# Kernel optimization log

Measured on AMD Instinct MI355X. Metric: run time of the kernel, lower is better.

## Reference

```python
import jax, jax.numpy as jnp
import numpy as np

B, T, S = 64, 128, 128
E, H, D, K = 512, 1024, 1024, 1024  # embed, hidden, decoder_size, encoder.output_size
IN2 = 2 * D + 2 * H  # output_rnn input size


def gru_cell(x, h, Wih, Whh, bih, bhh):
    # PyTorch GRUCell math; gate order (r, z, n)
    gi = x @ Wih.T + bih
    gh = h @ Whh.T + bhh
    i_r, i_z, i_n = jnp.split(gi, 3, axis=-1)
    h_r, h_z, h_n = jnp.split(gh, 3, axis=-1)
    r = jax.nn.sigmoid(i_r + h_r)
    z = jax.nn.sigmoid(i_z + h_z)
    n = jnp.tanh(i_n + r * h_n)
    return (1.0 - z) * n + z * h


def setup_inputs() -> dict:
    key = jax.random.key(0)
    ks = jax.random.split(key, 24)
    p = 0.05
    rn = lambda k, s, sc=1.0: jax.random.normal(k, s, jnp.float32) * sc
    return {
        'reversed_input': rn(ks[0], (B, T, E)),
        'y_length': jnp.full((B,), T, jnp.int32),
        'mask': jnp.ones((B, T), bool),
        'y_states': rn(ks[1], (B, T, D)),
        'encoder_output': rn(ks[2], (B, S, K)),
        'src_mask': jnp.ones((B, 1, S), bool),
        # backward-reading GRU (self.rnn)
        'rnn_Wih': rn(ks[3], (3 * H, E), p), 'rnn_Whh': rn(ks[4], (3 * H, H), p),
        'rnn_bih': rn(ks[5], (3 * H,), p), 'rnn_bhh': rn(ks[6], (3 * H,), p),
        # output_rnn GRU
        'out_Wih': rn(ks[7], (3 * H, IN2), p), 'out_Whh': rn(ks[8], (3 * H, H), p),
        'out_bih': rn(ks[9], (3 * H,), p), 'out_bhh': rn(ks[10], (3 * H,), p),
        'corr_W': rn(ks[11], (D, H), p), 'corr_b': rn(ks[12], (D,), p),
        'reward_W': rn(ks[13], (2, H), p), 'reward_b': rn(ks[14], (2,), p),
        'attv_W': rn(ks[15], (H, H + K), p), 'attv_b': rn(ks[16], (H,), p),
        # Bahdanau attention (bias-free linears)
        'key_W': rn(ks[17], (H, K), p), 'query_W': rn(ks[18], (H, H), p),
        'energy_W': rn(ks[19], (1, H), p),
    }


def reference(reversed_input, y_length, mask, y_states, encoder_output, src_mask,
              rnn_Wih, rnn_Whh, rnn_bih, rnn_bhh,
              out_Wih, out_Whh, out_bih, out_bhh,
              corr_W, corr_b, reward_W, reward_b,
              attv_W, attv_b, key_W, query_W, energy_W):
    b, t, _ = reversed_input.shape
    h_dim = rnn_Whh.shape[1]
    d_dim = corr_W.shape[0]
    dt = reversed_input.dtype

    # _apply_rnn: step-by-step GRU over reversed input == full GRU scan
    def rnn_step(h, x):
        h = gru_cell(x, h, rnn_Wih, rnn_Whh, rnn_bih, rnn_bhh)
        return h, h
    h0 = jnp.zeros((b, h_dim), dt)
    _, rnn_outs = jax.lax.scan(rnn_step, h0, reversed_input.transpose(1, 0, 2))
    rnn_outputs = jnp.flip(rnn_outs.transpose(1, 0, 2), axis=1)  # [B,T,H]

    proj_keys = encoder_output @ key_W.T  # [B,S,H] precomputed attention keys
    comb_states = jnp.concatenate([y_states, rnn_outputs], axis=-1)  # [B,T,D+H]
    sm = src_mask[:, 0, :]  # [B,S]

    def step(carry, comb_t):
        h, corr_prev, att_prev = carry
        inp = jnp.concatenate([comb_t, corr_prev, att_prev], axis=-1)  # [B,2D+2H]
        h = gru_cell(inp, h, out_Wih, out_Whh, out_bih, out_bhh)  # rnn_output == hidden[-1]
        corr = jnp.tanh(h @ corr_W.T + corr_b)  # corr_activation=tanh
        reward = h @ reward_W.T + reward_b  # [B,2]
        reward_pred = jax.lax.stop_gradient(jnp.argmax(reward, axis=-1)).astype(dt)[:, None]
        # Bahdanau attention: v^T tanh(Wq q + Wk k)
        pq = h @ query_W.T  # [B,H]
        energies = jnp.tanh(pq[:, None, :] + proj_keys) @ energy_W[0]  # [B,S]
        scores = jnp.where(sm, energies, -jnp.inf)
        alphas = jax.nn.softmax(scores, axis=-1)
        context = jnp.einsum('bs,bsk->bk', alphas, encoder_output)
        att_vec = jnp.tanh(jnp.concatenate([h, context], axis=-1) @ attv_W.T + attv_b)
        corr = corr * (1.0 - reward_pred)
        return (h, corr, att_vec), (corr, reward, alphas)

    init = (jnp.zeros((b, h_dim), dt), jnp.zeros((b, d_dim), dt), jnp.zeros((b, h_dim), dt))
    _, (corrs, rewards, attns) = jax.lax.scan(step, init, comb_states.transpose(1, 0, 2))
    return (corrs.transpose(1, 0, 2), rewards.transpose(1, 0, 2), attns.transpose(1, 0, 2))
```

## Files before the change

### kernel.cpp

```cpp
#include <hip/hip_runtime.h>
#include <hip/hip_bf16.h>
#include <math.h>

#define B 64
#define T 128
#define S 128
#define E 512
#define H 1024
#define D 1024
#define KDIM 1024
#define G3 3072
#define JT 16

__device__ __forceinline__ float sigmoidf_(float x) { return 1.f / (1.f + expf(-x)); }

template<int SRC>
__global__ __launch_bounds__(256) void gemm128(
    const float* __restrict__ A1, const float* __restrict__ A2, int lda,
    const float* __restrict__ W, int ldw, const float* __restrict__ bias,
    float* __restrict__ C, int ldc, int Kd, int c0, int chLog) {
  __shared__ __align__(16) float As[16][132];
  __shared__ __align__(16) float Ws[16][132];
  const int bm = blockIdx.y * 128;
  const int bn = blockIdx.x * 128;
  const int tid = threadIdx.x;
  const int tr = tid >> 4, tc = tid & 15;
  float acc[8][8];
#pragma unroll
  for (int i = 0; i < 8; ++i)
#pragma unroll
    for (int j = 0; j < 8; ++j) acc[i][j] = 0.f;

  for (int k0 = 0; k0 < Kd; k0 += 16) {
#pragma unroll
    for (int l = 0; l < 8; ++l) {
      int i = tid + l * 256;
      int r = i >> 4, kk = i & 15;
      int rg = bm + r;
      int k = k0 + kk;
      float v;
      if (SRC == 0) {
        v = A1[(size_t)rg * lda + k];
      } else {
        int b = rg >> chLog, tl = rg & ((1 << chLog) - 1);
        int trow = b * T + c0 + tl;
        if (SRC == 1) v = A1[(size_t)trow * E + k];
        else v = (k < 1024) ? A1[(size_t)trow * 1024 + k]
                            : A2[(size_t)trow * 1024 + (k - 1024)];
      }
      As[kk][r] = v;
    }
#pragma unroll
    for (int l = 0; l < 8; ++l) {
      int i = tid + l * 256;
      int c = i >> 4, kk = i & 15;
      Ws[kk][c] = W[(size_t)(bn + c) * ldw + k0 + kk];
    }
    __syncthreads();
#pragma unroll
    for (int kk = 0; kk < 16; ++kk) {
      float a[8], w[8];
      *(float4*)&a[0] = *(const float4*)&As[kk][tr * 8];
      *(float4*)&a[4] = *(const float4*)&As[kk][tr * 8 + 4];
      *(float4*)&w[0] = *(const float4*)&Ws[kk][tc * 8];
      *(float4*)&w[4] = *(const float4*)&Ws[kk][tc * 8 + 4];
#pragma unroll
      for (int i = 0; i < 8; ++i)
#pragma unroll
        for (int j = 0; j < 8; ++j)
          acc[i][j] = fmaf(a[i], w[j], acc[i][j]);
    }
    __syncthreads();
  }
#pragma unroll
  for (int i = 0; i < 8; ++i) {
    int rg = bm + tr * 8 + i;
#pragma unroll
    for (int j = 0; j < 8; ++j) {
      int cc = bn + tc * 8 + j;
      float bv = bias ? bias[cc] : 0.f;
      C[(size_t)rg * ldc + cc] = acc[i][j] + bv;
    }
  }
}

struct SBSeg { const float* A; const float* W; int lda; int ldw; int N; };
struct SBArgs { SBSeg s[6]; };

__global__ __launch_bounds__(256) void sb_gemm(SBArgs args, int jtPerSeg, int Nstr,
                                               float* __restrict__ part) {
  const int seg = blockIdx.x / jtPerSeg;
  const int jt = blockIdx.x % jtPerSeg;
  const SBSeg sg = args.s[seg];
  const int j0 = jt * JT;
  if (j0 >= sg.N) return;
  const int wv = __builtin_amdgcn_readfirstlane(threadIdx.x >> 6);
  const int lane = threadIdx.x & 63;
  float a[128];
  const float4* ap = (const float4*)(sg.A + (size_t)lane * sg.lda + wv * 128);
#pragma unroll
  for (int q = 0; q < 32; ++q) {
    float4 v = ap[q];
    a[q * 4 + 0] = v.x; a[q * 4 + 1] = v.y; a[q * 4 + 2] = v.z; a[q * 4 + 3] = v.w;
  }
  float acc[JT];
#pragma unroll
  for (int jj = 0; jj < JT; ++jj) acc[jj] = 0.f;
#pragma unroll
  for (int jj = 0; jj < JT; ++jj) {
    int j = j0 + jj;
    if (j < sg.N) {
      const float4* wp = (const float4*)(sg.W + (size_t)j * sg.ldw + wv * 128);
      float s0 = 0.f, s1 = 0.f, s2 = 0.f, s3 = 0.f;
#pragma unroll
      for (int q = 0; q < 32; ++q) {
        float4 w4 = wp[q];
        s0 = fmaf(a[q * 4 + 0], w4.x, s0);
        s1 = fmaf(a[q * 4 + 1], w4.y, s1);
        s2 = fmaf(a[q * 4 + 2], w4.z, s2);
        s3 = fmaf(a[q * 4 + 3], w4.w, s3);
      }
      acc[jj] = (s0 + s1) + (s2 + s3);
    }
  }
  __shared__ float red[4][JT][64];
#pragma unroll
  for (int jj = 0; jj < JT; ++jj) red[wv][jj][lane] = acc[jj];
  __syncthreads();
  for (int idx = threadIdx.x; idx < JT * 64; idx += 256) {
    int b = idx >> 4, jj = idx & 15;
    int j = j0 + jj;
    if (j < sg.N) {
      float v = red[0][jj][b] + red[1][jj][b] + red[2][jj][b] + red[3][jj][b];
      part[((size_t)seg * 64 + b) * Nstr + j] = v;
    }
  }
}

__global__ __launch_bounds__(256) void gru_reduce(
    const float* __restrict__ part, const float* __restrict__ gi,
    int CH, int tl, int nsGi, int ghStart, int nsGh,
    const float* __restrict__ bhh, float* __restrict__ hrow,
    float* __restrict__ flip_out, int t) {
  const int b = blockIdx.x >> 2;
  const int j = (blockIdx.x & 3) * 256 + threadIdx.x;
  const float* gb = gi + (size_t)(b * CH + tl) * G3;
  float gir = gb[j];
  float giz = gb[H + j];
  float gin = gb[2 * H + j];
  for (int p2 = 0; p2 < nsGi; ++p2) {
    const float* pp = part + ((size_t)p2 * 64 + b) * G3;
    gir += pp[j]; giz += pp[H + j]; gin += pp[2 * H + j];
  }
  float ghr = bhh[j], ghz = bhh[H + j], ghn = bhh[2 * H + j];
  for (int p2 = ghStart; p2 < ghStart + nsGh; ++p2) {
    const float* pp = part + ((size_t)p2 * 64 + b) * G3;
    ghr += pp[j]; ghz += pp[H + j]; ghn += pp[2 * H + j];
  }
  float r = sigmoidf_(gir + ghr);
  float z = sigmoidf_(giz + ghz);
  float n = tanhf(gin + r * ghn);
  float hold = hrow[(size_t)b * H + j];
  float hnew = (1.f - z) * n + z * hold;
  hrow[(size_t)b * H + j] = hnew;
  if (flip_out)
    flip_out[(size_t)b * T * H + (size_t)(T - 1 - t) * H + j] = hnew;
}

__global__ __launch_bounds__(256) void hproj_gemm(
    const float* __restrict__ h,
    const float* __restrict__ corrW, const float* __restrict__ corrB,
    const float* __restrict__ qW, const float* __restrict__ avW,
    const float* __restrict__ rewW, const float* __restrict__ rewB,
    float* __restrict__ corrR, float* __restrict__ pq,
    float* __restrict__ attH, float* __restrict__ rew,
    float* __restrict__ out_rewards, int t) {
  const int task = blockIdx.x;
  const int tid = threadIdx.x;
  const int wv = __builtin_amdgcn_readfirstlane(tid >> 6);
  const int lane = tid & 63;
  const float* Wb; int ldw = 1024, n0, nrows, typ;
  if (task < 128)      { Wb = corrW; n0 = task * 8;         nrows = 8; typ = 0; }
  else if (task < 256) { Wb = qW;    n0 = (task - 128) * 8; nrows = 8; typ = 1; }
  else if (task < 384) { Wb = avW;   n0 = (task - 256) * 8; nrows = 8; typ = 2; ldw = 2048; }
  else                 { Wb = rewW;  n0 = 0;                nrows = 2; typ = 3; }
  const int k0 = wv * 256;
  const float* arow = h + (size_t)lane * H + k0;
  float acc[8] = {0.f, 0.f, 0.f, 0.f, 0.f, 0.f, 0.f, 0.f};
  for (int sc = 0; sc < 8; ++sc) {
    float av[32];
    const float4* ap = (const float4*)(arow + sc * 32);
#pragma unroll
    for (int q = 0; q < 8; ++q) {
      float4 v = ap[q];
      av[4*q] = v.x; av[4*q+1] = v.y; av[4*q+2] = v.z; av[4*q+3] = v.w;
    }
#pragma unroll
    for (int rr = 0; rr < 8; ++rr) {
      if (rr < nrows) {
        const float4* wp = (const float4*)(Wb + (size_t)(n0 + rr) * ldw + k0 + sc * 32);
        float s = acc[rr];
#pragma unroll
        for (int q = 0; q < 8; ++q) {
          float4 w = wp[q];
          s = fmaf(av[4*q],   w.x, s);
          s = fmaf(av[4*q+1], w.y, s);
          s = fmaf(av[4*q+2], w.z, s);
          s = fmaf(av[4*q+3], w.w, s);
        }
        acc[rr] = s;
      }
    }
  }
  __shared__ float red[4][8][64];
#pragma unroll
  for (int rr = 0; rr < 8; ++rr) red[wv][rr][lane] = acc[rr];
  __syncthreads();
  for (int idx = tid; idx < 512; idx += 256) {
    int b = idx >> 3, jj = idx & 7;
    if (jj < nrows) {
      int n = n0 + jj;
      float v = red[0][jj][b] + red[1][jj][b] + red[2][jj][b] + red[3][jj][b];
      if (typ == 0) corrR[(size_t)b * 1024 + n] = v + corrB[n];
      else if (typ == 1) pq[(size_t)b * 1024 + n] = v;
      else if (typ == 2) attH[(size_t)n * 64 + b] = v;
      else {
        float rv = v + rewB[n];
        rew[n * 64 + b] = rv;
        out_rewards[((size_t)b * T + t) * 2 + n] = rv;
      }
    }
  }
}

__global__ __launch_bounds__(256) void energy_kernel(
    const float* __restrict__ pq, const float* __restrict__ pk,
    const float* __restrict__ eW, float* __restrict__ energies) {
  int wid = blockIdx.x * 4 + (threadIdx.x >> 6);
  int lane = threadIdx.x & 63;
  int b = wid >> 7, s = wid & 127;
  const float* pkp = pk + ((size_t)b * S + s) * H;
  const float* qp = pq + (size_t)b * H;
  float acc = 0.f;
#pragma unroll
  for (int i = 0; i < 16; ++i) {
    int j = lane + i * 64;
    acc += tanhf(qp[j] + pkp[j]) * eW[j];
  }
#pragma unroll
  for (int off = 32; off > 0; off >>= 1) acc += __shfl_down(acc, off);
  if (lane == 0) energies[b * S + s] = acc;
}

__global__ __launch_bounds__(256) void smct_plus(
    const float* __restrict__ energies, const float* __restrict__ enc,
    const float* __restrict__ corrR, const float* __restrict__ rew,
    float* __restrict__ ctx, float* __restrict__ uv,
    float* __restrict__ out_attns, float* __restrict__ out_corrs, int t) {
  int b = blockIdx.x, kt = blockIdx.y;
  int tid = threadIdx.x;
  __shared__ float se[128], sa[128], ss[128];
  if (tid < 128) { se[tid] = energies[b * S + tid]; sa[tid] = se[tid]; }
  __syncthreads();
  for (int st2 = 64; st2 > 0; st2 >>= 1) {
    if (tid < st2) sa[tid] = fmaxf(sa[tid], sa[tid + st2]);
    __syncthreads();
  }
  float mx = sa[0];
  __syncthreads();
  if (tid < 128) { sa[tid] = expf(se[tid] - mx); ss[tid] = sa[tid]; }
  __syncthreads();
  for (int st2 = 64; st2 > 0; st2 >>= 1) {
    if (tid < st2) ss[tid] += ss[tid + st2];
    __syncthreads();
  }
  float inv = 1.f / ss[0];
  __syncthreads();
  if (tid < 128) sa[tid] *= inv;
  __syncthreads();
  int k = kt * 256 + tid;
  const float* eb = enc + (size_t)b * S * KDIM + k;
  float acc = 0.f;
#pragma unroll 4
  for (int s2 = 0; s2 < S; ++s2) acc = fmaf(sa[s2], eb[(size_t)s2 * KDIM], acc);
  ctx[(size_t)b * KDIM + k] = acc;
  float r0 = rew[b], r1 = rew[64 + b];
  float g = (r1 > r0) ? 0.f : 1.f;
  float cv = g * tanhf(corrR[(size_t)b * 1024 + k]);
  uv[(size_t)b * 2048 + k] = cv;
  out_corrs[((size_t)b * T + t) * D + k] = cv;
  if (kt == 0 && tid < 128) out_attns[((size_t)b * T + t) * S + tid] = sa[tid];
}

__global__ __launch_bounds__(256) void final_attv(
    const float* __restrict__ attH, const float* __restrict__ avW,
    const float* __restrict__ avB, const float* __restrict__ ctx,
    float* __restrict__ uv) {
  const int n0 = blockIdx.x * 8;
  const int tid = threadIdx.x;
  const int wv = __builtin_amdgcn_readfirstlane(tid >> 6);
  const int lane = tid & 63;
  __shared__ float red[4][8][64];
  float acc[8];
#pragma unroll
  for (int jj = 0; jj < 8; ++jj) acc[jj] = 0.f;
  const int k0 = wv * 256;
  const float* arow = ctx + (size_t)lane * KDIM + k0;
  for (int sc = 0; sc < 8; ++sc) {
    float av[32];
    const float4* ap = (const float4*)(arow + sc * 32);
#pragma unroll
    for (int q = 0; q < 8; ++q) {
      float4 v = ap[q];
      av[4*q] = v.x; av[4*q+1] = v.y; av[4*q+2] = v.z; av[4*q+3] = v.w;
    }
#pragma unroll
    for (int jj = 0; jj < 8; ++jj) {
      const float4* wp = (const float4*)(avW + (size_t)(n0 + jj) * 2048 + 1024 + k0 + sc * 32);
      float s = acc[jj];
#pragma unroll
      for (int q = 0; q < 8; ++q) {
        float4 w = wp[q];
        s = fmaf(av[4*q],   w.x, s);
        s = fmaf(av[4*q+1], w.y, s);
        s = fmaf(av[4*q+2], w.z, s);
        s = fmaf(av[4*q+3], w.w, s);
      }
      acc[jj] = s;
    }
  }
#pragma unroll
  for (int jj = 0; jj < 8; ++jj) red[wv][jj][lane] = acc[jj];
  __syncthreads();
  for (int idx = tid; idx < 512; idx += 256) {
    int jj = idx >> 6, bb = idx & 63;
    int n = n0 + jj;
    float v = red[0][jj][bb] + red[1][jj][bb] + red[2][jj][bb] + red[3][jj][bb]
            + attH[(size_t)n * 64 + bb] + avB[n];
    uv[(size_t)bb * 2048 + 1024 + n] = tanhf(v);
  }
}

extern "C" void kernel_launch(void* const* d_in, const int* in_sizes, int n_in,
                              void* d_out, int out_size, void* d_ws, size_t ws_size,
                              hipStream_t stream) {
  const float* reversed_input = (const float*)d_in[0];
  const float* y_states = (const float*)d_in[3];
  const float* encoder = (const float*)d_in[4];
  const float* rnn_Wih = (const float*)d_in[6];
  const float* rnn_Whh = (const float*)d_in[7];
  const float* rnn_bih = (const float*)d_in[8];
  const float* rnn_bhh = (const float*)d_in[9];
  const float* out_Wih = (const float*)d_in[10];
  const float* out_Whh = (const float*)d_in[11];
  const float* out_bih = (const float*)d_in[12];
  const float* out_bhh = (const float*)d_in[13];
  const float* corr_W = (const float*)d_in[14];
  const float* corr_b = (const float*)d_in[15];
  const float* reward_W = (const float*)d_in[16];
  const float* reward_b = (const float*)d_in[17];
  const float* attv_W = (const float*)d_in[18];
  const float* attv_b = (const float*)d_in[19];
  const float* key_W = (const float*)d_in[20];
  const float* query_W = (const float*)d_in[21];
  const float* energy_W = (const float*)d_in[22];

  float* out_corrs = (float*)d_out;
  float* out_rewards = out_corrs + (size_t)B * T * D;
  float* out_attns = out_rewards + (size_t)B * T * 2;

  float* p = (float*)d_ws;
  float* rnn_flip = p;  p += (size_t)B * T * H;
  float* proj_keys = p; p += (size_t)B * S * H;
  float* part = p;      p += (size_t)6 * 64 * G3;
  float* h = p;         p += (size_t)B * H;
  float* uv = p;        p += (size_t)B * 2048;
  float* ctx = p;       p += (size_t)B * KDIM;
  float* corrR = p;     p += (size_t)B * 1024;
  float* pq = p;        p += (size_t)B * H;
  float* attH = p;      p += (size_t)H * 64;
  float* rew = p;       p += 128;
  float* energ = p;     p += (size_t)B * S;
  size_t fixedF = (size_t)(p - (float*)d_ws);
  int CH = 8, chLog = 3;
  {
    int c = 64, l = 6;
    for (; c >= 8; c >>= 1, --l)
      if (ws_size >= (fixedF + (size_t)c * 64 * G3) * 4) break;
    if (c < 8) { c = 8; l = 3; }
    CH = c; chLog = l;
  }
  float* gibuf = p;

  hipMemsetAsync(h, 0, (size_t)B * H * sizeof(float), stream);
  hipMemsetAsync(uv, 0, (size_t)B * 2048 * sizeof(float), stream);

  dim3 blk(256);

  gemm128<0><<<dim3(H / 128, (B * S) / 128), blk, 0, stream>>>(
      encoder, nullptr, KDIM, key_W, KDIM, nullptr, proj_keys, H, KDIM, 0, 0);

  for (int c0 = 0; c0 < T; c0 += CH) {
    gemm128<1><<<dim3(G3 / 128, (64 * CH) / 128), blk, 0, stream>>>(
        reversed_input, nullptr, 0, rnn_Wih, E, rnn_bih, gibuf, G3, E, c0, chLog);
    for (int tl = 0; tl < CH; ++tl) {
      int t = c0 + tl;
      SBArgs s1{};
      s1.s[0] = { h, rnn_Whh, H, H, G3 };
      s1.s[1] = { h + 512, rnn_Whh + 512, H, H, G3 };
      sb_gemm<<<2 * 192, blk, 0, stream>>>(s1, 192, G3, part);
      gru_reduce<<<256, blk, 0, stream>>>(part, gibuf, CH, tl, 0, 0, 2,
                                          rnn_bhh, h, rnn_flip, t);
    }
  }

  hipMemsetAsync(h, 0, (size_t)B * H * sizeof(float), stream);
  for (int c0 = 0; c0 < T; c0 += CH) {
    gemm128<2><<<dim3(G3 / 128, (64 * CH) / 128), blk, 0, stream>>>(
        y_states, rnn_flip, 0, out_Wih, 4096, out_bih, gibuf, G3, 2048, c0, chLog);
    for (int tl = 0; tl < CH; ++tl) {
      int t = c0 + tl;
      SBArgs k1{};
      for (int s2 = 0; s2 < 4; ++s2)
        k1.s[s2] = { uv + s2 * 512, out_Wih + 2048 + s2 * 512, 2048, 4096, G3 };
      for (int s2 = 0; s2 < 2; ++s2)
        k1.s[4 + s2] = { h + s2 * 512, out_Whh + s2 * 512, H, H, G3 };
      sb_gemm<<<6 * 192, blk, 0, stream>>>(k1, 192, G3, part);
      gru_reduce<<<256, blk, 0, stream>>>(part, gibuf, CH, tl, 4, 4, 2,
                                          out_bhh, h, nullptr, t);
      hproj_gemm<<<385, blk, 0, stream>>>(h, corr_W, corr_b, query_W, attv_W,
                                          reward_W, reward_b, corrR, pq, attH,
                                          rew, out_rewards, t);
      energy_kernel<<<2048, blk, 0, stream>>>(pq, proj_keys, energy_W, energ);
      smct_plus<<<dim3(B, 4), blk, 0, stream>>>(energ, encoder, corrR, rew,
                                                ctx, uv, out_attns, out_corrs, t);
      final_attv<<<128, blk, 0, stream>>>(attH, attv_W, attv_b, ctx, uv);
    }
  }
}
```

Baseline: 23.03 ms.

## Fuse GRU reduction and softmax-context into producer kernels via last-block atomics

Merges the split-K recurrent GEMM with the GRU gate reduction in one kernel. An atomic counter per column group lets the last finishing block compute the gates, and the hidden state is double-buffered to avoid read/write races. The energy kernel and the softmax/context kernel are fused the same way, with a per-batch counter. This removes two launches per timestep. In exchange, the final reduction and the context computation now run on only a few blocks (one per batch row for context), so that tail work is serialized.

```diff
diff --git a/kernel.cpp b/kernel.cpp
--- a/kernel.cpp
+++ b/kernel.cpp
@@ -84,87 +84,100 @@
   }
 }
 
-struct SBSeg { const float* A; const float* W; int lda; int ldw; int N; };
-struct SBArgs { SBSeg s[6]; };
-
-__global__ __launch_bounds__(256) void sb_gemm(SBArgs args, int jtPerSeg, int Nstr,
-                                               float* __restrict__ part) {
-  const int seg = blockIdx.x / jtPerSeg;
-  const int jt = blockIdx.x % jtPerSeg;
-  const SBSeg sg = args.s[seg];
+struct SBSeg { const float* A; const float* W; int lda; int ldw; };
+struct FGArgs {
+  SBSeg s[6];
+  int nseg;
+  int nsGi;
+  const float* gi;
+  int CH; int tl;
+  const float* bhh;
+  const float* hprev;
+  float* hcur;
+  float* flip;
+  int t;
+  float* part;
+  unsigned int* cnt;
+};
+
+__global__ __launch_bounds__(256) void sbg_gru(FGArgs a) {
+  const int seg = blockIdx.x / 192;
+  const int jt = blockIdx.x % 192;
+  const SBSeg sg = a.s[seg];
   const int j0 = jt * JT;
-  if (j0 >= sg.N) return;
-  const int wv = __builtin_amdgcn_readfirstlane(threadIdx.x >> 6);
-  const int lane = threadIdx.x & 63;
-  float a[128];
+  const int tid = threadIdx.x;
+  const int wv = __builtin_amdgcn_readfirstlane(tid >> 6);
+  const int lane = tid & 63;
+  float av[128];
   const float4* ap = (const float4*)(sg.A + (size_t)lane * sg.lda + wv * 128);
 #pragma unroll
   for (int q = 0; q < 32; ++q) {
     float4 v = ap[q];
-    a[q * 4 + 0] = v.x; a[q * 4 + 1] = v.y; a[q * 4 + 2] = v.z; a[q * 4 + 3] = v.w;
+    av[q * 4 + 0] = v.x; av[q * 4 + 1] = v.y; av[q * 4 + 2] = v.z; av[q * 4 + 3] = v.w;
   }
   float acc[JT];
 #pragma unroll
   for (int jj = 0; jj < JT; ++jj) acc[jj] = 0.f;
 #pragma unroll
   for (int jj = 0; jj < JT; ++jj) {
-    int j = j0 + jj;
-    if (j < sg.N) {
-      const float4* wp = (const float4*)(sg.W + (size_t)j * sg.ldw + wv * 128);
-      float s0 = 0.f, s1 = 0.f, s2 = 0.f, s3 = 0.f;
-#pragma unroll
-      for (int q = 0; q < 32; ++q) {
-        float4 w4 = wp[q];
-        s0 = fmaf(a[q * 4 + 0], w4.x, s0);
-        s1 = fmaf(a[q * 4 + 1], w4.y, s1);
-        s2 = fmaf(a[q * 4 + 2], w4.z, s2);
-        s3 = fmaf(a[q * 4 + 3], w4.w, s3);
-      }
-      acc[jj] = (s0 + s1) + (s2 + s3);
-    }
+    const float4* wp = (const float4*)(sg.W + (size_t)(j0 + jj) * sg.ldw + wv * 128);
+    float s0 = 0.f, s1 = 0.f, s2 = 0.f, s3 = 0.f;
+#pragma unroll
+    for (int q = 0; q < 32; ++q) {
+      float4 w4 = wp[q];
+      s0 = fmaf(av[q * 4 + 0], w4.x, s0);
+      s1 = fmaf(av[q * 4 + 1], w4.y, s1);
+      s2 = fmaf(av[q * 4 + 2], w4.z, s2);
+      s3 = fmaf(av[q * 4 + 3], w4.w, s3);
+    }
+    acc[jj] = (s0 + s1) + (s2 + s3);
   }
   __shared__ float red[4][JT][64];
 #pragma unroll
   for (int jj = 0; jj < JT; ++jj) red[wv][jj][lane] = acc[jj];
   __syncthreads();
-  for (int idx = threadIdx.x; idx < JT * 64; idx += 256) {
+  for (int idx = tid; idx < JT * 64; idx += 256) {
     int b = idx >> 4, jj = idx & 15;
-    int j = j0 + jj;
-    if (j < sg.N) {
-      float v = red[0][jj][b] + red[1][jj][b] + red[2][jj][b] + red[3][jj][b];
-      part[((size_t)seg * 64 + b) * Nstr + j] = v;
-    }
-  }
-}
-
-__global__ __launch_bounds__(256) void gru_reduce(
-    const float* __restrict__ part, const float* __restrict__ gi,
-    int CH, int tl, int nsGi, int ghStart, int nsGh,
-    const float* __restrict__ bhh, float* __restrict__ hrow,
-    float* __restrict__ flip_out, int t) {
-  const int b = blockIdx.x >> 2;
-  const int j = (blockIdx.x & 3) * 256 + threadIdx.x;
-  const float* gb = gi + (size_t)(b * CH + tl) * G3;
-  float gir = gb[j];
-  float giz = gb[H + j];
-  float gin = gb[2 * H + j];
-  for (int p2 = 0; p2 < nsGi; ++p2) {
-    const float* pp = part + ((size_t)p2 * 64 + b) * G3;
-    gir += pp[j]; giz += pp[H + j]; gin += pp[2 * H + j];
-  }
-  float ghr = bhh[j], ghz = bhh[H + j], ghn = bhh[2 * H + j];
-  for (int p2 = ghStart; p2 < ghStart + nsGh; ++p2) {
-    const float* pp = part + ((size_t)p2 * 64 + b) * G3;
-    ghr += pp[j]; ghz += pp[H + j]; ghn += pp[2 * H + j];
-  }
-  float r = sigmoidf_(gir + ghr);
-  float z = sigmoidf_(giz + ghz);
-  float n = tanhf(gin + r * ghn);
-  float hold = hrow[(size_t)b * H + j];
-  float hnew = (1.f - z) * n + z * hold;
-  hrow[(size_t)b * H + j] = hnew;
-  if (flip_out)
-    flip_out[(size_t)b * T * H + (size_t)(T - 1 - t) * H + j] = hnew;
+    float v = red[0][jj][b] + red[1][jj][b] + red[2][jj][b] + red[3][jj][b];
+    a.part[((size_t)seg * 64 + b) * G3 + j0 + jj] = v;
+  }
+  __threadfence();
+  __syncthreads();
+  __shared__ int isLast;
+  if (tid == 0) {
+    int grp = jt & 63;
+    unsigned int old = atomicAdd(&a.cnt[grp], 1u);
+    isLast = (old == (unsigned)(a.nseg * 3 - 1)) ? 1 : 0;
+    if (isLast) a.cnt[grp] = 0;
+  }
+  __syncthreads();
+  if (!isLast) return;
+  __threadfence();
+  const int grp = jt & 63;
+  const int jg0 = grp * 16;
+  for (int idx = tid; idx < 1024; idx += 256) {
+    int b = idx >> 4, jj = idx & 15;
+    int j = jg0 + jj;
+    const float* gb = a.gi + (size_t)(b * a.CH + a.tl) * G3;
+    float gir = gb[j], giz = gb[H + j], gin = gb[2 * H + j];
+    for (int p2 = 0; p2 < a.nsGi; ++p2) {
+      const float* pp = a.part + ((size_t)p2 * 64 + b) * G3;
+      gir += pp[j]; giz += pp[H + j]; gin += pp[2 * H + j];
+    }
+    float ghr = a.bhh[j], ghz = a.bhh[H + j], ghn = a.bhh[2 * H + j];
+    for (int p2 = a.nsGi; p2 < a.nseg; ++p2) {
+      const float* pp = a.part + ((size_t)p2 * 64 + b) * G3;
+      ghr += pp[j]; ghz += pp[H + j]; ghn += pp[2 * H + j];
+    }
+    float r = sigmoidf_(gir + ghr);
+    float z = sigmoidf_(giz + ghz);
+    float n = tanhf(gin + r * ghn);
+    float hold = a.hprev[(size_t)b * H + j];
+    float hnew = (1.f - z) * n + z * hold;
+    a.hcur[(size_t)b * H + j] = hnew;
+    if (a.flip)
+      a.flip[(size_t)b * T * H + (size_t)(T - 1 - a.t) * H + j] = hnew;
+  }
 }
 
 __global__ __launch_bounds__(256) void hproj_gemm(
@@ -233,34 +246,45 @@
   }
 }
 
-__global__ __launch_bounds__(256) void energy_kernel(
+__global__ __launch_bounds__(256) void energy_smct(
     const float* __restrict__ pq, const float* __restrict__ pk,
-    const float* __restrict__ eW, float* __restrict__ energies) {
-  int wid = blockIdx.x * 4 + (threadIdx.x >> 6);
-  int lane = threadIdx.x & 63;
-  int b = wid >> 7, s = wid & 127;
-  const float* pkp = pk + ((size_t)b * S + s) * H;
-  const float* qp = pq + (size_t)b * H;
-  float acc = 0.f;
-#pragma unroll
-  for (int i = 0; i < 16; ++i) {
-    int j = lane + i * 64;
-    acc += tanhf(qp[j] + pkp[j]) * eW[j];
-  }
-#pragma unroll
-  for (int off = 32; off > 0; off >>= 1) acc += __shfl_down(acc, off);
-  if (lane == 0) energies[b * S + s] = acc;
-}
-
-__global__ __launch_bounds__(256) void smct_plus(
-    const float* __restrict__ energies, const float* __restrict__ enc,
+    const float* __restrict__ eW, const float* __restrict__ enc,
     const float* __restrict__ corrR, const float* __restrict__ rew,
     float* __restrict__ ctx, float* __restrict__ uv,
+    float* __restrict__ energ, unsigned int* __restrict__ cnt,
     float* __restrict__ out_attns, float* __restrict__ out_corrs, int t) {
-  int b = blockIdx.x, kt = blockIdx.y;
-  int tid = threadIdx.x;
-  __shared__ float se[128], sa[128], ss[128];
-  if (tid < 128) { se[tid] = energies[b * S + tid]; sa[tid] = se[tid]; }
+  const int tid = threadIdx.x;
+  const int wv = tid >> 6, lane = tid & 63;
+  const int wid = blockIdx.x * 4 + wv;
+  const int b = blockIdx.x >> 5;
+  {
+    const int s = wid & 127;
+    const float* pkp = pk + ((size_t)b * S + s) * H;
+    const float* qp = pq + (size_t)b * H;
+    float acc = 0.f;
+#pragma unroll
+    for (int i = 0; i < 16; ++i) {
+      int j = lane + i * 64;
+      acc += tanhf(qp[j] + pkp[j]) * eW[j];
+    }
+#pragma unroll
+    for (int off = 32; off > 0; off >>= 1) acc += __shfl_down(acc, off);
+    if (lane == 0) energ[b * S + s] = acc;
+  }
+  __threadfence();
+  __syncthreads();
+  __shared__ int isLast;
+  if (tid == 0) {
+    unsigned int old = atomicAdd(&cnt[b], 1u);
+    isLast = (old == 31u) ? 1 : 0;
+    if (isLast) cnt[b] = 0;
+  }
+  __syncthreads();
+  if (!isLast) return;
+  __threadfence();
+  __shared__ float sa[128], ss[128];
+  float ev = 0.f;
+  if (tid < 128) { ev = energ[b * S + tid]; sa[tid] = ev; }
   __syncthreads();
   for (int st2 = 64; st2 > 0; st2 >>= 1) {
     if (tid < st2) sa[tid] = fmaxf(sa[tid], sa[tid + st2]);
@@ -268,7 +292,8 @@
   }
   float mx = sa[0];
   __syncthreads();
-  if (tid < 128) { sa[tid] = expf(se[tid] - mx); ss[tid] = sa[tid]; }
+  float e2 = 0.f;
+  if (tid < 128) { e2 = expf(ev - mx); sa[tid] = e2; ss[tid] = e2; }
   __syncthreads();
   for (int st2 = 64; st2 > 0; st2 >>= 1) {
     if (tid < st2) ss[tid] += ss[tid + st2];
@@ -276,20 +301,26 @@
   }
   float inv = 1.f / ss[0];
   __syncthreads();
-  if (tid < 128) sa[tid] *= inv;
-  __syncthreads();
-  int k = kt * 256 + tid;
-  const float* eb = enc + (size_t)b * S * KDIM + k;
-  float acc = 0.f;
-#pragma unroll 4
-  for (int s2 = 0; s2 < S; ++s2) acc = fmaf(sa[s2], eb[(size_t)s2 * KDIM], acc);
-  ctx[(size_t)b * KDIM + k] = acc;
+  if (tid < 128) {
+    float a2 = e2 * inv;
+    sa[tid] = a2;
+    out_attns[((size_t)b * T + t) * S + tid] = a2;
+  }
+  __syncthreads();
   float r0 = rew[b], r1 = rew[64 + b];
   float g = (r1 > r0) ? 0.f : 1.f;
-  float cv = g * tanhf(corrR[(size_t)b * 1024 + k]);
-  uv[(size_t)b * 2048 + k] = cv;
-  out_corrs[((size_t)b * T + t) * D + k] = cv;
-  if (kt == 0 && tid < 128) out_attns[((size_t)b * T + t) * S + tid] = sa[tid];
+#pragma unroll
+  for (int kq = 0; kq < 4; ++kq) {
+    int k = kq * 256 + tid;
+    const float* eb = enc + (size_t)b * S * KDIM + k;
+    float acc = 0.f;
+#pragma unroll 4
+    for (int s2 = 0; s2 < S; ++s2) acc = fmaf(sa[s2], eb[(size_t)s2 * KDIM], acc);
+    ctx[(size_t)b * KDIM + k] = acc;
+    float cv = g * tanhf(corrR[(size_t)b * 1024 + k]);
+    uv[(size_t)b * 2048 + k] = cv;
+    out_corrs[((size_t)b * T + t) * D + k] = cv;
+  }
 }
 
 __global__ __launch_bounds__(256) void final_attv(
@@ -373,7 +404,8 @@
   float* rnn_flip = p;  p += (size_t)B * T * H;
   float* proj_keys = p; p += (size_t)B * S * H;
   float* part = p;      p += (size_t)6 * 64 * G3;
-  float* h = p;         p += (size_t)B * H;
+  float* hA = p;        p += (size_t)B * H;
+  float* hB = p;        p += (size_t)B * H;
   float* uv = p;        p += (size_t)B * 2048;
   float* ctx = p;       p += (size_t)B * KDIM;
   float* corrR = p;     p += (size_t)B * 1024;
@@ -381,6 +413,8 @@
   float* attH = p;      p += (size_t)H * 64;
   float* rew = p;       p += 128;
   float* energ = p;     p += (size_t)B * S;
+  unsigned int* cntG = (unsigned int*)p; p += 64;
+  unsigned int* cntB = (unsigned int*)p; p += 64;
   size_t fixedF = (size_t)(p - (float*)d_ws);
   int CH = 8, chLog = 3;
   {
@@ -392,8 +426,9 @@
   }
   float* gibuf = p;
 
-  hipMemsetAsync(h, 0, (size_t)B * H * sizeof(float), stream);
+  hipMemsetAsync(hA, 0, (size_t)B * H * sizeof(float), stream);
   hipMemsetAsync(uv, 0, (size_t)B * 2048 * sizeof(float), stream);
+  hipMemsetAsync(cntG, 0, 128 * sizeof(unsigned int), stream);
 
   dim3 blk(256);
 
@@ -405,35 +440,45 @@
         reversed_input, nullptr, 0, rnn_Wih, E, rnn_bih, gibuf, G3, E, c0, chLog);
     for (int tl = 0; tl < CH; ++tl) {
       int t = c0 + tl;
-      SBArgs s1{};
-      s1.s[0] = { h, rnn_Whh, H, H, G3 };
-      s1.s[1] = { h + 512, rnn_Whh + 512, H, H, G3 };
-      sb_gemm<<<2 * 192, blk, 0, stream>>>(s1, 192, G3, part);
-      gru_reduce<<<256, blk, 0, stream>>>(part, gibuf, CH, tl, 0, 0, 2,
-                                          rnn_bhh, h, rnn_flip, t);
-    }
-  }
-
-  hipMemsetAsync(h, 0, (size_t)B * H * sizeof(float), stream);
+      const float* hp_ = (t & 1) ? hB : hA;
+      float* hc_ = (t & 1) ? hA : hB;
+      FGArgs fa{};
+      fa.s[0] = { hp_, rnn_Whh, H, H };
+      fa.s[1] = { hp_ + 512, rnn_Whh + 512, H, H };
+      fa.nseg = 2; fa.nsGi = 0;
+      fa.gi = gibuf; fa.CH = CH; fa.tl = tl;
+      fa.bhh = rnn_bhh; fa.hprev = hp_; fa.hcur = hc_;
+      fa.flip = rnn_flip; fa.t = t;
+      fa.part = part; fa.cnt = cntG;
+      sbg_gru<<<2 * 192, blk, 0, stream>>>(fa);
+    }
+  }
+
+  hipMemsetAsync(hA, 0, (size_t)B * H * sizeof(float), stream);
   for (int c0 = 0; c0 < T; c0 += CH) {
     gemm128<2><<<dim3(G3 / 128, (64 * CH) / 128), blk, 0, stream>>>(
         y_states, rnn_flip, 0, out_Wih, 4096, out_bih, gibuf, G3, 2048, c0, chLog);
     for (int tl = 0; tl < CH; ++tl) {
       int t = c0 + tl;
-      SBArgs k1{};
+      const float* hp_ = (t & 1) ? hB : hA;
+      float* hc_ = (t & 1) ? hA : hB;
+      FGArgs fa{};
       for (int s2 = 0; s2 < 4; ++s2)
-        k1.s[s2] = { uv + s2 * 512, out_Wih + 2048 + s2 * 512, 2048, 4096, G3 };
+        fa.s[s2] = { uv + s2 * 512, out_Wih + 2048 + s2 * 512, 2048, 4096 };
       for (int s2 = 0; s2 < 2; ++s2)
-        k1.s[4 + s2] = { h + s2 * 512, out_Whh + s2 * 512, H, H, G3 };
-      sb_gemm<<<6 * 192, blk, 0, stream>>>(k1, 192, G3, part);
-      gru_reduce<<<256, blk, 0, stream>>>(part, gibuf, CH, tl, 4, 4, 2,
-                                          out_bhh, h, nullptr, t);
-      hproj_gemm<<<385, blk, 0, stream>>>(h, corr_W, corr_b, query_W, attv_W,
+        fa.s[4 + s2] = { hp_ + s2 * 512, out_Whh + s2 * 512, H, H };
+      fa.nseg = 6; fa.nsGi = 4;
+      fa.gi = gibuf; fa.CH = CH; fa.tl = tl;
+      fa.bhh = out_bhh; fa.hprev = hp_; fa.hcur = hc_;
+      fa.flip = nullptr; fa.t = t;
+      fa.part = part; fa.cnt = cntG;
+      sbg_gru<<<6 * 192, blk, 0, stream>>>(fa);
+      hproj_gemm<<<385, blk, 0, stream>>>(hc_, corr_W, corr_b, query_W, attv_W,
                                           reward_W, reward_b, corrR, pq, attH,
                                           rew, out_rewards, t);
-      energy_kernel<<<2048, blk, 0, stream>>>(pq, proj_keys, energy_W, energ);
-      smct_plus<<<dim3(B, 4), blk, 0, stream>>>(energ, encoder, corrR, rew,
-                                                ctx, uv, out_attns, out_corrs, t);
+      energy_smct<<<2048, blk, 0, stream>>>(pq, proj_keys, energy_W, encoder,
+                                            corrR, rew, ctx, uv, energ, cntB,
+                                            out_attns, out_corrs, t);
       final_attv<<<128, blk, 0, stream>>>(attH, attv_W, attv_b, ctx, uv);
     }
   }
```

New measurement: 68.73 ms. +198.5%, slower.

## Fuse first GRU matvec with gate update; merge energy into attention kernel

Applied to the files above, without the earlier changes.

The backward-reading GRU step now runs as a single 512-thread kernel that computes h@Whh for four hidden units across all batches, reduces across waves in shared memory, and applies the gate math directly. It ping-pongs between two hidden-state buffers, which replaces the two launches and the partial-sum round trip through global memory. The energy computation is folded into the softmax/context kernel, dropping a launch and the energies buffer. The cost is that each of the 4 k-slice blocks per batch now recomputes all 128 energies redundantly, and the fused GRU kernel reads Whh with less parallelism per block.

```diff
diff --git a/kernel.cpp b/kernel.cpp
--- a/kernel.cpp
+++ b/kernel.cpp
@@ -81,6 +81,75 @@
       float bv = bias ? bias[cc] : 0.f;
       C[(size_t)rg * ldc + cc] = acc[i][j] + bv;
     }
+  }
+}
+
+struct G1Args {
+  const float* gi; const float* Whh; const float* bhh;
+  const float* hprev; float* hcur; float* flip;
+  int CH; int tl; int t;
+};
+
+__global__ __launch_bounds__(512) void fused_g1(G1Args a) {
+  const int j0 = blockIdx.x * 4;
+  const int tid = threadIdx.x;
+  const int wv = tid >> 6, lane = tid & 63;
+  __shared__ float red[8][12][64];
+  __shared__ float st[4][64];
+  float acc[12];
+#pragma unroll
+  for (int r = 0; r < 12; ++r) acc[r] = 0.f;
+  for (int p = 0; p < 2; ++p) {
+    const int k0 = (p * 8 + wv) * 64;
+    float av[64];
+    const float4* ap = (const float4*)(a.hprev + (size_t)lane * H + k0);
+#pragma unroll
+    for (int q = 0; q < 16; ++q) {
+      float4 v = ap[q];
+      av[4*q] = v.x; av[4*q+1] = v.y; av[4*q+2] = v.z; av[4*q+3] = v.w;
+    }
+#pragma unroll
+    for (int jj = 0; jj < 4; ++jj)
+#pragma unroll
+      for (int g = 0; g < 3; ++g) {
+        const float4* wp = (const float4*)(a.Whh + (size_t)(g * H + j0 + jj) * H + k0);
+        float s = acc[jj * 3 + g];
+#pragma unroll
+        for (int q = 0; q < 16; ++q) {
+          float4 w = wp[q];
+          s = fmaf(av[4*q],   w.x, s);
+          s = fmaf(av[4*q+1], w.y, s);
+          s = fmaf(av[4*q+2], w.z, s);
+          s = fmaf(av[4*q+3], w.w, s);
+        }
+        acc[jj * 3 + g] = s;
+      }
+  }
+#pragma unroll
+  for (int r = 0; r < 12; ++r) red[wv][r][lane] = acc[r];
+  __syncthreads();
+  if (tid < 256) {
+    const int jj = tid >> 6, b = tid & 63, j = j0 + jj;
+    float ghr = a.bhh[j], ghz = a.bhh[H + j], ghn = a.bhh[2 * H + j];
+#pragma unroll
+    for (int w = 0; w < 8; ++w) {
+      ghr += red[w][jj * 3 + 0][b];
+      ghz += red[w][jj * 3 + 1][b];
+      ghn += red[w][jj * 3 + 2][b];
+    }
+    const float* gb = a.gi + (size_t)(b * a.CH + a.tl) * G3;
+    float r = sigmoidf_(gb[j] + ghr);
+    float z = sigmoidf_(gb[H + j] + ghz);
+    float n = tanhf(gb[2 * H + j] + r * ghn);
+    float hnew = (1.f - z) * n + z * a.hprev[(size_t)b * H + j];
+    st[jj][b] = hnew;
+  }
+  __syncthreads();
+  if (tid < 256) {
+    const int jl = tid & 3, b2 = tid >> 2;
+    float v = st[jl][b2];
+    a.hcur[(size_t)b2 * H + j0 + jl] = v;
+    a.flip[(size_t)b2 * T * H + (size_t)(T - 1 - a.t) * H + j0 + jl] = v;
   }
 }
 
@@ -233,34 +302,37 @@
   }
 }
 
-__global__ __launch_bounds__(256) void energy_kernel(
+__global__ __launch_bounds__(256) void attn_slice(
     const float* __restrict__ pq, const float* __restrict__ pk,
-    const float* __restrict__ eW, float* __restrict__ energies) {
-  int wid = blockIdx.x * 4 + (threadIdx.x >> 6);
-  int lane = threadIdx.x & 63;
-  int b = wid >> 7, s = wid & 127;
-  const float* pkp = pk + ((size_t)b * S + s) * H;
-  const float* qp = pq + (size_t)b * H;
-  float acc = 0.f;
-#pragma unroll
-  for (int i = 0; i < 16; ++i) {
-    int j = lane + i * 64;
-    acc += tanhf(qp[j] + pkp[j]) * eW[j];
-  }
-#pragma unroll
-  for (int off = 32; off > 0; off >>= 1) acc += __shfl_down(acc, off);
-  if (lane == 0) energies[b * S + s] = acc;
-}
-
-__global__ __launch_bounds__(256) void smct_plus(
-    const float* __restrict__ energies, const float* __restrict__ enc,
+    const float* __restrict__ eW, const float* __restrict__ enc,
     const float* __restrict__ corrR, const float* __restrict__ rew,
     float* __restrict__ ctx, float* __restrict__ uv,
     float* __restrict__ out_attns, float* __restrict__ out_corrs, int t) {
-  int b = blockIdx.x, kt = blockIdx.y;
-  int tid = threadIdx.x;
+  const int b = blockIdx.x;
+  const int ks = blockIdx.y;
+  const int tid = threadIdx.x;
+  const int s = tid & 127, half = tid >> 7;
+  __shared__ float ep[2][128];
   __shared__ float se[128], sa[128], ss[128];
-  if (tid < 128) { se[tid] = energies[b * S + tid]; sa[tid] = se[tid]; }
+  {
+    const float4* qp = (const float4*)(pq + (size_t)b * H + half * 512);
+    const float4* pkp = (const float4*)(pk + ((size_t)b * S + s) * H + half * 512);
+    const float4* ewp = (const float4*)(eW + half * 512);
+    float acc = 0.f;
+#pragma unroll 4
+    for (int q = 0; q < 128; ++q) {
+      float4 qv = qp[q];
+      float4 kv = pkp[q];
+      float4 evv = ewp[q];
+      acc += tanhf(qv.x + kv.x) * evv.x;
+      acc += tanhf(qv.y + kv.y) * evv.y;
+      acc += tanhf(qv.z + kv.z) * evv.z;
+      acc += tanhf(qv.w + kv.w) * evv.w;
+    }
+    ep[half][s] = acc;
+  }
+  __syncthreads();
+  if (tid < 128) { float e = ep[0][tid] + ep[1][tid]; se[tid] = e; sa[tid] = e; }
   __syncthreads();
   for (int st2 = 64; st2 > 0; st2 >>= 1) {
     if (tid < st2) sa[tid] = fmaxf(sa[tid], sa[tid + st2]);
@@ -268,7 +340,7 @@
   }
   float mx = sa[0];
   __syncthreads();
-  if (tid < 128) { sa[tid] = expf(se[tid] - mx); ss[tid] = sa[tid]; }
+  if (tid < 128) { float e2 = expf(se[tid] - mx); sa[tid] = e2; ss[tid] = e2; }
   __syncthreads();
   for (int st2 = 64; st2 > 0; st2 >>= 1) {
     if (tid < st2) ss[tid] += ss[tid + st2];
@@ -278,7 +350,8 @@
   __syncthreads();
   if (tid < 128) sa[tid] *= inv;
   __syncthreads();
-  int k = kt * 256 + tid;
+  if (ks == 0 && tid < 128) out_attns[((size_t)b * T + t) * S + tid] = sa[tid];
+  const int k = ks * 256 + tid;
   const float* eb = enc + (size_t)b * S * KDIM + k;
   float acc = 0.f;
 #pragma unroll 4
@@ -289,7 +362,6 @@
   float cv = g * tanhf(corrR[(size_t)b * 1024 + k]);
   uv[(size_t)b * 2048 + k] = cv;
   out_corrs[((size_t)b * T + t) * D + k] = cv;
-  if (kt == 0 && tid < 128) out_attns[((size_t)b * T + t) * S + tid] = sa[tid];
 }
 
 __global__ __launch_bounds__(256) void final_attv(
@@ -373,14 +445,14 @@
   float* rnn_flip = p;  p += (size_t)B * T * H;
   float* proj_keys = p; p += (size_t)B * S * H;
   float* part = p;      p += (size_t)6 * 64 * G3;
-  float* h = p;         p += (size_t)B * H;
+  float* hA = p;        p += (size_t)B * H;
+  float* hB = p;        p += (size_t)B * H;
   float* uv = p;        p += (size_t)B * 2048;
   float* ctx = p;       p += (size_t)B * KDIM;
   float* corrR = p;     p += (size_t)B * 1024;
   float* pq = p;        p += (size_t)B * H;
   float* attH = p;      p += (size_t)H * 64;
   float* rew = p;       p += 128;
-  float* energ = p;     p += (size_t)B * S;
   size_t fixedF = (size_t)(p - (float*)d_ws);
   int CH = 8, chLog = 3;
   {
@@ -392,10 +464,10 @@
   }
   float* gibuf = p;
 
-  hipMemsetAsync(h, 0, (size_t)B * H * sizeof(float), stream);
+  hipMemsetAsync(hA, 0, (size_t)B * H * sizeof(float), stream);
   hipMemsetAsync(uv, 0, (size_t)B * 2048 * sizeof(float), stream);
 
-  dim3 blk(256);
+  dim3 blk(256), blk512(512);
 
   gemm128<0><<<dim3(H / 128, (B * S) / 128), blk, 0, stream>>>(
       encoder, nullptr, KDIM, key_W, KDIM, nullptr, proj_keys, H, KDIM, 0, 0);
@@ -405,16 +477,16 @@
         reversed_input, nullptr, 0, rnn_Wih, E, rnn_bih, gibuf, G3, E, c0, chLog);
     for (int tl = 0; tl < CH; ++tl) {
       int t = c0 + tl;
-      SBArgs s1{};
-      s1.s[0] = { h, rnn_Whh, H, H, G3 };
-      s1.s[1] = { h + 512, rnn_Whh + 512, H, H, G3 };
-      sb_gemm<<<2 * 192, blk, 0, stream>>>(s1, 192, G3, part);
-      gru_reduce<<<256, blk, 0, stream>>>(part, gibuf, CH, tl, 0, 0, 2,
-                                          rnn_bhh, h, rnn_flip, t);
-    }
-  }
-
-  hipMemsetAsync(h, 0, (size_t)B * H * sizeof(float), stream);
+      G1Args g1;
+      g1.gi = gibuf; g1.Whh = rnn_Whh; g1.bhh = rnn_bhh;
+      g1.hprev = (t & 1) ? hB : hA;
+      g1.hcur = (t & 1) ? hA : hB;
+      g1.flip = rnn_flip; g1.CH = CH; g1.tl = tl; g1.t = t;
+      fused_g1<<<256, blk512, 0, stream>>>(g1);
+    }
+  }
+
+  hipMemsetAsync(hA, 0, (size_t)B * H * sizeof(float), stream);
   for (int c0 = 0; c0 < T; c0 += CH) {
     gemm128<2><<<dim3(G3 / 128, (64 * CH) / 128), blk, 0, stream>>>(
         y_states, rnn_flip, 0, out_Wih, 4096, out_bih, gibuf, G3, 2048, c0, chLog);
@@ -424,16 +496,16 @@
       for (int s2 = 0; s2 < 4; ++s2)
         k1.s[s2] = { uv + s2 * 512, out_Wih + 2048 + s2 * 512, 2048, 4096, G3 };
       for (int s2 = 0; s2 < 2; ++s2)
-        k1.s[4 + s2] = { h + s2 * 512, out_Whh + s2 * 512, H, H, G3 };
+        k1.s[4 + s2] = { hA + s2 * 512, out_Whh + s2 * 512, H, H, G3 };
       sb_gemm<<<6 * 192, blk, 0, stream>>>(k1, 192, G3, part);
       gru_reduce<<<256, blk, 0, stream>>>(part, gibuf, CH, tl, 4, 4, 2,
-                                          out_bhh, h, nullptr, t);
-      hproj_gemm<<<385, blk, 0, stream>>>(h, corr_W, corr_b, query_W, attv_W,
+                                          out_bhh, hA, nullptr, t);
+      hproj_gemm<<<385, blk, 0, stream>>>(hA, corr_W, corr_b, query_W, attv_W,
                                           reward_W, reward_b, corrR, pq, attH,
                                           rew, out_rewards, t);
-      energy_kernel<<<2048, blk, 0, stream>>>(pq, proj_keys, energy_W, energ);
-      smct_plus<<<dim3(B, 4), blk, 0, stream>>>(energ, encoder, corrR, rew,
-                                                ctx, uv, out_attns, out_corrs, t);
+      attn_slice<<<dim3(B, 4), blk, 0, stream>>>(pq, proj_keys, energy_W, encoder,
+                                                 corrR, rew, ctx, uv,
+                                                 out_attns, out_corrs, t);
       final_attv<<<128, blk, 0, stream>>>(attH, attv_W, attv_b, ctx, uv);
     }
   }
```

Result: slower. 31.40 ms (+36.3%).
